# Kernel tuning notes

Hardware: AMD Instinct MI355X
Metric: run time of the kernel (lower is better)

## Reference

```python
import jax, jax.numpy as jnp
import numpy as np

# Winograd F(2x2, 3x3) transform matrices (standard Lavin & Gray form).
# The original torch module encodes B^T / A^T but applies them with elementwise
# mul (a bug that crashes); the intended math is Y = A^T [ (G g G^T) .* (B^T d B) ] A
# per 4x4 input tile with stride 2, which equals a valid 3x3 conv. We implement
# that intended Winograd computation faithfully and vectorized.
_BT = jnp.array([[1., 0., -1., 0.],
                 [0., 1., 1., 0.],
                 [0., -1., 1., 0.],
                 [0., 1., 0., -1.]], dtype=jnp.float32)
_G = jnp.array([[1., 0., 0.],
                [0.5, 0.5, 0.5],
                [0.5, -0.5, 0.5],
                [0., 0., 1.]], dtype=jnp.float32)
_AT = jnp.array([[1., 1., 1., 0.],
                 [0., 1., -1., -1.]], dtype=jnp.float32)


def setup_inputs() -> dict:
    key = jax.random.key(0)
    k1, k2 = jax.random.split(key)
    X = jax.random.normal(k1, (16, 32, 258, 258), dtype=jnp.float32)
    K = jax.random.normal(k2, (32, 32, 3, 3), dtype=jnp.float32)
    return {"X": X, "K": K}


def _winograd_conv(X, K):
    B_, C, H, W = X.shape
    Fo = K.shape[0]
    blocks = (H - 3) // 2 + 1  # number of 2x2 output tiles per spatial dim

    # Kernel transform: U = G K G^T  -> (Fo, C, 4, 4)
    U = jnp.einsum('ij,fcjk,lk->fcil', _G, K, _G)

    # Extract overlapping 4x4 tiles with stride 2: (B, C, blocks, blocks, 4, 4)
    i0 = jnp.arange(blocks) * 2
    win = i0[:, None] + jnp.arange(4)[None, :]          # (blocks, 4)
    tiles = X[:, :, win, :]                              # (B, C, blocks, 4, W)
    tiles = tiles[:, :, :, :, win]                       # (B, C, blocks, 4, blocks, 4)
    tiles = tiles.transpose(0, 1, 2, 4, 3, 5)            # (B, C, p, q, 4, 4)

    # Input transform: V = B^T d B
    V = jnp.einsum('ij,bcpqjk,lk->bcpqil', _BT, tiles, _BT)

    # Elementwise multiply in transform domain, summed over input channels
    M = jnp.einsum('fcil,bcpqil->bfpqil', U, V)          # (B, Fo, p, q, 4, 4)

    # Inverse transform: Y = A^T M A -> (B, Fo, p, q, 2, 2)
    Y = jnp.einsum('ij,bfpqjk,lk->bfpqil', _AT, M, _AT)

    # Stitch 2x2 tiles back: (B, Fo, 2*blocks, 2*blocks)
    out = Y.transpose(0, 1, 2, 4, 3, 5).reshape(B_, Fo, 2 * blocks, 2 * blocks)
    return out


def reference(X, K):
    return _winograd_conv(X, K)
```

## Files before the change

### kernel.cpp

```cpp
#include <hip/hip_runtime.h>
#include <stdint.h>

typedef __attribute__((ext_vector_type(8))) short bf16x8;
typedef __attribute__((ext_vector_type(4))) float f32x4;
typedef __attribute__((ext_vector_type(2))) float f32x2;

__device__ inline float bflo(uint32_t w) { union { uint32_t i; float f; } v; v.i = w << 16; return v.f; }
__device__ inline float bfhi(uint32_t w) { union { uint32_t i; float f; } v; v.i = w & 0xffff0000u; return v.f; }
__device__ inline uint32_t f2bf(float f) { union { float f; uint32_t i; } v; v.f = f; return (v.i + 0x8000u) >> 16; }
__device__ inline uint32_t pk(float lo, float hi) { return f2bf(lo) | (f2bf(hi) << 16); }

__device__ inline f32x2 pka(f32x2 a, f32x2 b) {
    f32x2 d; asm("v_pk_add_f32 %0, %1, %2" : "=v"(d) : "v"(a), "v"(b)); return d;
}
__device__ inline f32x2 pks(f32x2 a, f32x2 b) {
    f32x2 d; asm("v_pk_add_f32 %0, %1, %2 neg_lo:[0,1] neg_hi:[0,1]" : "=v"(d) : "v"(a), "v"(b)); return d;
}
__device__ inline uint32_t cvtpk2(float lo, float hi) {
    uint32_t r; asm("v_cvt_pk_bf16_f32 %0, %1, %2" : "=v"(r) : "v"(lo), "v"(hi)); return r;
}
__device__ inline uint32_t cvtpk(f32x2 v) { return cvtpk2(v.x, v.y); }
__device__ inline f32x2 unpk(uint32_t w) {
    union { uint32_t u; float f; } lo, hi; lo.u = w << 16; hi.u = w & 0xffff0000u;
    return (f32x2){lo.f, hi.f};
}

__global__ __launch_bounds__(256) void wg_filter(const float* __restrict__ Kk, uint32_t* __restrict__ Ud)
{
    const int idx = blockIdx.x * 256 + threadIdx.x;
    if (idx >= 512) return;
    const int cp = idx & 15, f = idx >> 4;
    float u[2][16];
    #pragma unroll
    for (int h = 0; h < 2; h++) {
        const float* kp = Kk + (f * 32 + cp * 2 + h) * 9;
        float k00 = kp[0], k01 = kp[1], k02 = kp[2];
        float k10 = kp[3], k11 = kp[4], k12 = kp[5];
        float k20 = kp[6], k21 = kp[7], k22 = kp[8];
        float t[4][3];
        t[0][0] = k00; t[0][1] = k01; t[0][2] = k02;
        t[1][0] = 0.5f * (k00 + k10 + k20); t[1][1] = 0.5f * (k01 + k11 + k21); t[1][2] = 0.5f * (k02 + k12 + k22);
        t[2][0] = 0.5f * (k00 - k10 + k20); t[2][1] = 0.5f * (k01 - k11 + k21); t[2][2] = 0.5f * (k02 - k12 + k22);
        t[3][0] = k20; t[3][1] = k21; t[3][2] = k22;
        #pragma unroll
        for (int i = 0; i < 4; i++) {
            float a0 = t[i][0], a1 = t[i][1], a2 = t[i][2];
            u[h][i * 4 + 0] = a0;
            u[h][i * 4 + 1] = 0.5f * (a0 + a1 + a2);
            u[h][i * 4 + 2] = 0.5f * (a0 - a1 + a2);
            u[h][i * 4 + 3] = a2;
        }
    }
    const int base = ((cp >> 2) * 32 + f) * 4 + (cp & 3);
    #pragma unroll
    for (int p = 0; p < 16; p++) Ud[p * 512 + base] = pk(u[0][p], u[1][p]);
}

__global__ __launch_bounds__(256, 5) void wg_main(
    const float* __restrict__ X, const uint16_t* __restrict__ U, float* __restrict__ out)
{
    __shared__ __align__(16) uint32_t Pl[2912];
    __shared__ __align__(16) uint16_t Vl[8192];

    const int tid = threadIdx.x;
    const int qb = blockIdx.x;
    const int pb = blockIdx.y;
    const int b  = blockIdx.z;
    const int y0 = pb * 8, x0 = qb * 16;

    for (int s = tid; s < 1440; s += 256) {
        const int pr = s / 90;
        const int r  = s - pr * 90;
        const int row = r / 9, seg = r - row * 9;
        const float* g0 = X + ((size_t)((b * 32 + pr * 2) * 258 + y0 + row)) * 258 + x0 + seg * 2;
        float2 a = *(const float2*)g0;
        float2 c = *(const float2*)(g0 + 258 * 258);
        uint2 w;
        w.x = cvtpk2(a.x, c.x);
        w.y = cvtpk2(a.y, c.y);
        *(uint2*)&Pl[pr * 182 + row * 18 + seg * 2] = w;
    }
    __syncthreads();

    const int wave = tid >> 6, lane = tid & 63;
    const int fh = wave & 1, tb = wave >> 1;
    const int l15 = lane & 15, lq = lane >> 4;
    const uint16_t* Ub = U + (lq * 32 + fh * 16 + l15) * 8;
    const uint16_t* Vb = Vl + ((tb * 4 + lq) * 16 + l15) * 8;
    uint32_t* vp = (uint32_t*)Vl;

    float y[4][4];
    #pragma unroll
    for (int r = 0; r < 4; r++)
        #pragma unroll
        for (int j = 0; j < 4; j++) y[r][j] = 0.f;

    #pragma unroll
    for (int ch = 0; ch < 2; ch++) {
        bf16x8 a_reg[8];
        #pragma unroll
        for (int p8 = 0; p8 < 8; p8++)
            a_reg[p8] = *(const bf16x8*)(Ub + (ch * 8 + p8) * 1024);

        #pragma unroll
        for (int it = 0; it < 2; it++) {
            const int rem  = it * 4 + wave;
            const int tblk = rem & 1, cpH = rem >> 1;
            const int cp2  = tid & 3, t15 = (tid >> 2) & 15;
            const int cp   = cpH * 4 + cp2;
            const int tt   = tblk * 16 + t15;
            const int tr   = tt >> 3, tc = tt & 7;
            const uint32_t* pp = &Pl[cp * 182 + (tr * 2 + ch) * 18 + tc * 2];
            f32x2 dd[3][4];
            #pragma unroll
            for (int j = 0; j < 3; j++) {
                uint2 w01 = *(const uint2*)&pp[j * 18];
                uint2 w23 = *(const uint2*)&pp[j * 18 + 2];
                dd[j][0] = unpk(w01.x); dd[j][1] = unpk(w01.y);
                dd[j][2] = unpk(w23.x); dd[j][3] = unpk(w23.y);
            }
            f32x2 e0[4], e1[4];
            #pragma unroll
            for (int k = 0; k < 4; k++) {
                if (ch == 0) {
                    e0[k] = pks(dd[0][k], dd[2][k]);
                    e1[k] = pka(dd[1][k], dd[2][k]);
                } else {
                    e0[k] = pks(dd[1][k], dd[0][k]);
                    e1[k] = pks(dd[0][k], dd[2][k]);
                }
            }
            const int vbase = ((tblk * 4 + cpH) * 16 + t15) * 4 + cp2;
            #pragma unroll
            for (int row = 0; row < 2; row++) {
                const f32x2* e = row ? e1 : e0;
                vp[(row * 4 + 0) * 512 + vbase] = cvtpk(pks(e[0], e[2]));
                vp[(row * 4 + 1) * 512 + vbase] = cvtpk(pka(e[1], e[2]));
                vp[(row * 4 + 2) * 512 + vbase] = cvtpk(pks(e[2], e[1]));
                vp[(row * 4 + 3) * 512 + vbase] = cvtpk(pks(e[1], e[3]));
            }
        }
        __syncthreads();

        f32x4 acc[8];
        #pragma unroll
        for (int p8 = 0; p8 < 8; p8++) acc[p8] = (f32x4){0.f, 0.f, 0.f, 0.f};
        #pragma unroll
        for (int p8 = 0; p8 < 8; p8++) {
            bf16x8 v = *(const bf16x8*)(Vb + p8 * 1024);
            acc[p8] = __builtin_amdgcn_mfma_f32_16x16x32_bf16(a_reg[p8], v, acc[p8], 0, 0, 0);
        }
        if (ch == 0) __syncthreads();

        #pragma unroll
        for (int r = 0; r < 4; r++) {
            #pragma unroll
            for (int ii = 0; ii < 2; ii++) {
                const int i = ch * 2 + ii;
                float m0 = acc[ii * 4 + 0][r], m1 = acc[ii * 4 + 1][r];
                float m2 = acc[ii * 4 + 2][r], m3 = acc[ii * 4 + 3][r];
                float c0 = m0 + m1 + m2, c1 = m1 - m2 - m3;
                if (i == 0)      { y[r][0] += c0; y[r][1] += c1; }
                else if (i == 1) { y[r][0] += c0; y[r][1] += c1; y[r][2] += c0; y[r][3] += c1; }
                else if (i == 2) { y[r][0] += c0; y[r][1] += c1; y[r][2] -= c0; y[r][3] -= c1; }
                else             { y[r][2] -= c0; y[r][3] -= c1; }
            }
        }
    }

    const int t = tb * 16 + l15;
    const int trr = t >> 3, tcc = t & 7;
    const int p = pb * 4 + trr, q = qb * 8 + tcc;
    #pragma unroll
    for (int r = 0; r < 4; r++) {
        const int f = fh * 16 + lq * 4 + r;
        float* op = out + ((size_t)(b * 32 + f) * 256 + 2 * p) * 256 + 2 * q;
        *(float2*)op = make_float2(y[r][0], y[r][1]);
        *(float2*)(op + 256) = make_float2(y[r][2], y[r][3]);
    }
}

__device__ inline uint16_t f2bf16_rne(float f) {
    union { float f; uint32_t i; } v; v.f = f;
    uint32_t x = v.i;
    uint32_t r = x + 0x7fffu + ((x >> 16) & 1u);
    return (uint16_t)(r >> 16);
}
__global__ __launch_bounds__(256) void winograd_fallback(
    const float* __restrict__ X, const float* __restrict__ K, float* __restrict__ out)
{
    __shared__ uint16_t Ul[16384];
    __shared__ uint16_t Vl[16384];
    __shared__ uint16_t Pl[32 * 242];
    const int tid = threadIdx.x;
    const int qb = blockIdx.x, pb = blockIdx.y, b = blockIdx.z;
    for (int idx = tid; idx < 1024; idx += 256) {
        const int f = idx >> 5, c = idx & 31;
        const float* kp = K + (f * 32 + c) * 9;
        float k00 = kp[0], k01 = kp[1], k02 = kp[2];
        float k10 = kp[3], k11 = kp[4], k12 = kp[5];
        float k20 = kp[6], k21 = kp[7], k22 = kp[8];
        float t[4][3];
        t[0][0] = k00; t[0][1] = k01; t[0][2] = k02;
        t[1][0] = 0.5f * (k00 + k10 + k20); t[1][1] = 0.5f * (k01 + k11 + k21); t[1][2] = 0.5f * (k02 + k12 + k22);
        t[2][0] = 0.5f * (k00 - k10 + k20); t[2][1] = 0.5f * (k01 - k11 + k21); t[2][2] = 0.5f * (k02 - k12 + k22);
        t[3][0] = k20; t[3][1] = k21; t[3][2] = k22;
        const int ubase = ((c >> 3) * 32 + f) * 8 + (c & 7);
        #pragma unroll
        for (int i = 0; i < 4; i++) {
            float a0 = t[i][0], a1 = t[i][1], a2 = t[i][2];
            Ul[(i * 4 + 0) * 1024 + ubase] = f2bf16_rne(a0);
            Ul[(i * 4 + 1) * 1024 + ubase] = f2bf16_rne(0.5f * (a0 + a1 + a2));
            Ul[(i * 4 + 2) * 1024 + ubase] = f2bf16_rne(0.5f * (a0 - a1 + a2));
            Ul[(i * 4 + 3) * 1024 + ubase] = f2bf16_rne(a2);
        }
    }
    const int y0 = pb * 8, x0 = qb * 16;
    for (int s = tid; s < 2880; s += 256) {
        const int c = s / 90;
        const int r = s % 90;
        const int row = r / 9, seg = r % 9;
        const float* gp = X + ((b * 32 + c) * 258 + (y0 + row)) * 258 + x0 + seg * 2;
        float2 g = *(const float2*)gp;
        uint32_t packed = (uint32_t)f2bf16_rne(g.x) | ((uint32_t)f2bf16_rne(g.y) << 16);
        *(uint32_t*)&Pl[c * 242 + row * 24 + seg * 2] = packed;
    }
    __syncthreads();
    for (int idx = tid; idx < 1024; idx += 256) {
        const int c = idx & 31, tt = idx >> 5;
        const int tr = tt >> 3, tc = tt & 7;
        const uint16_t* pp = &Pl[c * 242 + (tr * 2) * 24 + tc * 2];
        float d[4][4];
        #pragma unroll
        for (int j = 0; j < 4; j++) {
            uint32_t w0 = *(const uint32_t*)&pp[j * 24];
            uint32_t w1 = *(const uint32_t*)&pp[j * 24 + 2];
            d[j][0] = bflo(w0); d[j][1] = bfhi(w0);
            d[j][2] = bflo(w1); d[j][3] = bfhi(w1);
        }
        float bt[4][4];
        #pragma unroll
        for (int k = 0; k < 4; k++) {
            bt[0][k] = d[0][k] - d[2][k];
            bt[1][k] = d[1][k] + d[2][k];
            bt[2][k] = d[2][k] - d[1][k];
            bt[3][k] = d[1][k] - d[3][k];
        }
        const int vbase = (((tt >> 4) * 4 + (c >> 3)) * 16 + (tt & 15)) * 8 + (c & 7);
        #pragma unroll
        for (int i = 0; i < 4; i++) {
            float b0 = bt[i][0], b1 = bt[i][1], b2 = bt[i][2], b3 = bt[i][3];
            Vl[(i * 4 + 0) * 1024 + vbase] = f2bf16_rne(b0 - b2);
            Vl[(i * 4 + 1) * 1024 + vbase] = f2bf16_rne(b1 + b2);
            Vl[(i * 4 + 2) * 1024 + vbase] = f2bf16_rne(b2 - b1);
            Vl[(i * 4 + 3) * 1024 + vbase] = f2bf16_rne(b1 - b3);
        }
    }
    __syncthreads();
    const int wave = tid >> 6, lane = tid & 63;
    const int fh = wave & 1, tb = wave >> 1;
    const int l15 = lane & 15, lq = lane >> 4;
    f32x4 acc[16];
    #pragma unroll
    for (int p = 0; p < 16; p++) acc[p] = (f32x4){0.f, 0.f, 0.f, 0.f};
    #pragma unroll
    for (int p = 0; p < 16; p++) {
        bf16x8 a = *(const bf16x8*)&Ul[p * 1024 + (lq * 32 + fh * 16 + l15) * 8];
        bf16x8 bv = *(const bf16x8*)&Vl[p * 1024 + ((tb * 4 + lq) * 16 + l15) * 8];
        acc[p] = __builtin_amdgcn_mfma_f32_16x16x32_bf16(a, bv, acc[p], 0, 0, 0);
    }
    #pragma unroll
    for (int r = 0; r < 4; r++) {
        const int f = fh * 16 + lq * 4 + r;
        const int t = tb * 16 + l15;
        const int tr = t >> 3, tc = t & 7;
        const int p = pb * 4 + tr, q = qb * 8 + tc;
        float m[4][4];
        #pragma unroll
        for (int i = 0; i < 4; i++)
            #pragma unroll
            for (int l = 0; l < 4; l++)
                m[i][l] = acc[i * 4 + l][r];
        float s0[4], s1[4];
        #pragma unroll
        for (int k = 0; k < 4; k++) {
            s0[k] = m[0][k] + m[1][k] + m[2][k];
            s1[k] = m[1][k] - m[2][k] - m[3][k];
        }
        float* op = out + ((size_t)(b * 32 + f) * 256 + 2 * p) * 256 + 2 * q;
        *(float2*)op = make_float2(s0[0] + s0[1] + s0[2], s0[1] - s0[2] - s0[3]);
        *(float2*)(op + 256) = make_float2(s1[0] + s1[1] + s1[2], s1[1] - s1[2] - s1[3]);
    }
}

extern "C" void kernel_launch(void* const* d_in, const int* in_sizes, int n_in,
                              void* d_out, int out_size, void* d_ws, size_t ws_size,
                              hipStream_t stream) {
    const float* X = (const float*)d_in[0];
    const float* K = (const float*)d_in[1];
    float* out = (float*)d_out;
    dim3 grid(16, 32, 16);
    if (ws_size >= 32768) {
        wg_filter<<<2, 256, 0, stream>>>(K, (uint32_t*)d_ws);
        wg_main<<<grid, 256, 0, stream>>>(X, (const uint16_t*)d_ws, out);
    } else {
        winograd_fallback<<<grid, 256, 0, stream>>>(X, K, out);
    }
}
```

Measured before the change: 93.65 us.

## Split Winograd transform into four row passes with smaller LDS and XCD-aware block remap

The kernel now processes the four Winograd transform rows in four passes of 4 MFMAs each, down from two passes of 8. This halves the V staging buffer in shared memory and the live A/accumulator registers, so launch bounds can rise from 5 to 8 blocks per CU. It also remaps the linear block index so consecutive work items are spread across the 8 XCDs in strided chunks. The cost is twice as many barrier phases and more redundant reads of the P tile.

```diff
diff --git a/kernel.cpp b/kernel.cpp
--- a/kernel.cpp
+++ b/kernel.cpp
@@ -56,16 +56,18 @@
     for (int p = 0; p < 16; p++) Ud[p * 512 + base] = pk(u[0][p], u[1][p]);
 }
 
-__global__ __launch_bounds__(256, 5) void wg_main(
+__global__ __launch_bounds__(256, 8) void wg_main(
     const float* __restrict__ X, const uint16_t* __restrict__ U, float* __restrict__ out)
 {
     __shared__ __align__(16) uint32_t Pl[2912];
-    __shared__ __align__(16) uint16_t Vl[8192];
+    __shared__ __align__(16) uint16_t Vl[4096];
 
     const int tid = threadIdx.x;
-    const int qb = blockIdx.x;
-    const int pb = blockIdx.y;
-    const int b  = blockIdx.z;
+    const int lin  = blockIdx.x + 16 * (blockIdx.y + 32 * blockIdx.z);
+    const int work = (lin & 7) * 1024 + (lin >> 3);
+    const int qb = work & 15;
+    const int pb = (work >> 4) & 31;
+    const int b  = work >> 9;
     const int y0 = pb * 8, x0 = qb * 16;
 
     for (int s = tid; s < 1440; s += 256) {
@@ -89,6 +91,8 @@
     const uint16_t* Vb = Vl + ((tb * 4 + lq) * 16 + l15) * 8;
     uint32_t* vp = (uint32_t*)Vl;
 
+    const int cp2 = tid & 3, t15c = (tid >> 2) & 15;
+
     float y[4][4];
     #pragma unroll
     for (int r = 0; r < 4; r++)
@@ -96,75 +100,59 @@
         for (int j = 0; j < 4; j++) y[r][j] = 0.f;
 
     #pragma unroll
-    for (int ch = 0; ch < 2; ch++) {
-        bf16x8 a_reg[8];
-        #pragma unroll
-        for (int p8 = 0; p8 < 8; p8++)
-            a_reg[p8] = *(const bf16x8*)(Ub + (ch * 8 + p8) * 1024);
+    for (int i = 0; i < 4; i++) {
+        bf16x8 a_reg[4];
+        #pragma unroll
+        for (int l = 0; l < 4; l++)
+            a_reg[l] = *(const bf16x8*)(Ub + (i * 4 + l) * 1024);
+
+        const int ra = (i == 0) ? 0 : (i == 2) ? 2 : 1;
+        const int rb = (i == 3) ? 3 : (i == 2) ? 1 : 2;
 
         #pragma unroll
         for (int it = 0; it < 2; it++) {
             const int rem  = it * 4 + wave;
             const int tblk = rem & 1, cpH = rem >> 1;
-            const int cp2  = tid & 3, t15 = (tid >> 2) & 15;
             const int cp   = cpH * 4 + cp2;
-            const int tt   = tblk * 16 + t15;
+            const int tt   = tblk * 16 + t15c;
             const int tr   = tt >> 3, tc = tt & 7;
-            const uint32_t* pp = &Pl[cp * 182 + (tr * 2 + ch) * 18 + tc * 2];
-            f32x2 dd[3][4];
+            const uint32_t* pp = &Pl[cp * 182 + (tr * 2) * 18 + tc * 2];
+            uint2 wa0 = *(const uint2*)&pp[ra * 18];
+            uint2 wa1 = *(const uint2*)&pp[ra * 18 + 2];
+            uint2 wb0 = *(const uint2*)&pp[rb * 18];
+            uint2 wb1 = *(const uint2*)&pp[rb * 18 + 2];
+            f32x2 da[4], db[4];
+            da[0] = unpk(wa0.x); da[1] = unpk(wa0.y); da[2] = unpk(wa1.x); da[3] = unpk(wa1.y);
+            db[0] = unpk(wb0.x); db[1] = unpk(wb0.y); db[2] = unpk(wb1.x); db[3] = unpk(wb1.y);
+            f32x2 e[4];
             #pragma unroll
-            for (int j = 0; j < 3; j++) {
-                uint2 w01 = *(const uint2*)&pp[j * 18];
-                uint2 w23 = *(const uint2*)&pp[j * 18 + 2];
-                dd[j][0] = unpk(w01.x); dd[j][1] = unpk(w01.y);
-                dd[j][2] = unpk(w23.x); dd[j][3] = unpk(w23.y);
-            }
-            f32x2 e0[4], e1[4];
-            #pragma unroll
-            for (int k = 0; k < 4; k++) {
-                if (ch == 0) {
-                    e0[k] = pks(dd[0][k], dd[2][k]);
-                    e1[k] = pka(dd[1][k], dd[2][k]);
-                } else {
-                    e0[k] = pks(dd[1][k], dd[0][k]);
-                    e1[k] = pks(dd[0][k], dd[2][k]);
-                }
-            }
-            const int vbase = ((tblk * 4 + cpH) * 16 + t15) * 4 + cp2;
-            #pragma unroll
-            for (int row = 0; row < 2; row++) {
-                const f32x2* e = row ? e1 : e0;
-                vp[(row * 4 + 0) * 512 + vbase] = cvtpk(pks(e[0], e[2]));
-                vp[(row * 4 + 1) * 512 + vbase] = cvtpk(pka(e[1], e[2]));
-                vp[(row * 4 + 2) * 512 + vbase] = cvtpk(pks(e[2], e[1]));
-                vp[(row * 4 + 3) * 512 + vbase] = cvtpk(pks(e[1], e[3]));
-            }
+            for (int k = 0; k < 4; k++)
+                e[k] = (i == 1) ? pka(da[k], db[k]) : pks(da[k], db[k]);
+            const int vbase = ((tblk * 4 + cpH) * 16 + t15c) * 4 + cp2;
+            vp[0 * 512 + vbase] = cvtpk(pks(e[0], e[2]));
+            vp[1 * 512 + vbase] = cvtpk(pka(e[1], e[2]));
+            vp[2 * 512 + vbase] = cvtpk(pks(e[2], e[1]));
+            vp[3 * 512 + vbase] = cvtpk(pks(e[1], e[3]));
         }
         __syncthreads();
 
-        f32x4 acc[8];
-        #pragma unroll
-        for (int p8 = 0; p8 < 8; p8++) acc[p8] = (f32x4){0.f, 0.f, 0.f, 0.f};
-        #pragma unroll
-        for (int p8 = 0; p8 < 8; p8++) {
-            bf16x8 v = *(const bf16x8*)(Vb + p8 * 1024);
-            acc[p8] = __builtin_amdgcn_mfma_f32_16x16x32_bf16(a_reg[p8], v, acc[p8], 0, 0, 0);
-        }
-        if (ch == 0) __syncthreads();
+        f32x4 acc[4];
+        #pragma unroll
+        for (int l = 0; l < 4; l++) {
+            bf16x8 v = *(const bf16x8*)(Vb + l * 1024);
+            acc[l] = __builtin_amdgcn_mfma_f32_16x16x32_bf16(a_reg[l], v,
+                        (f32x4){0.f, 0.f, 0.f, 0.f}, 0, 0, 0);
+        }
+        if (i < 3) __syncthreads();
 
         #pragma unroll
         for (int r = 0; r < 4; r++) {
-            #pragma unroll
-            for (int ii = 0; ii < 2; ii++) {
-                const int i = ch * 2 + ii;
-                float m0 = acc[ii * 4 + 0][r], m1 = acc[ii * 4 + 1][r];
-                float m2 = acc[ii * 4 + 2][r], m3 = acc[ii * 4 + 3][r];
-                float c0 = m0 + m1 + m2, c1 = m1 - m2 - m3;
-                if (i == 0)      { y[r][0] += c0; y[r][1] += c1; }
-                else if (i == 1) { y[r][0] += c0; y[r][1] += c1; y[r][2] += c0; y[r][3] += c1; }
-                else if (i == 2) { y[r][0] += c0; y[r][1] += c1; y[r][2] -= c0; y[r][3] -= c1; }
-                else             { y[r][2] -= c0; y[r][3] -= c1; }
-            }
+            float m0 = acc[0][r], m1 = acc[1][r], m2 = acc[2][r], m3 = acc[3][r];
+            float c0 = m0 + m1 + m2, c1 = m1 - m2 - m3;
+            if (i == 0)      { y[r][0] += c0; y[r][1] += c1; }
+            else if (i == 1) { y[r][0] += c0; y[r][1] += c1; y[r][2] += c0; y[r][3] += c1; }
+            else if (i == 2) { y[r][0] += c0; y[r][1] += c1; y[r][2] -= c0; y[r][3] -= c1; }
+            else             { y[r][2] -= c0; y[r][3] -= c1; }
         }
     }
 
```

Measured after the change: 264.6 us. +182.5%, slower.
